# Kernel tuning notes

Hardware: AMD Instinct MI355X
Metric: run time of the kernel (lower is better)

The kernel has to match this reference:

```python
import math
import jax, jax.numpy as jnp
import numpy as np

B, T, D = 4, 2048, 1024
H = 16
HD = D // H  # 64

def setup_inputs() -> dict:
    key = jax.random.key(0)
    k1, k2, k3 = jax.random.split(key, 3)
    x = jax.random.normal(k1, (B, T, D), dtype=jnp.float32)
    # weights stored as [in, out]; equivalent to torch Linear weight [out,in] transposed
    w_qkv = jax.random.normal(k2, (D, 3 * D), dtype=jnp.float32) * (1.0 / math.sqrt(D))
    w_out = jax.random.normal(k3, (D, D), dtype=jnp.float32) * (1.0 / math.sqrt(D))
    return {"x": x, "w_qkv": w_qkv, "w_out": w_out}

def reference(x, w_qkv, w_out):
    b, t, c = x.shape
    hd = c // H
    qkv = x @ w_qkv                                   # [B,T,3C]
    q, k, v = jnp.split(qkv, 3, axis=-1)
    # [B,T,C] -> [B,H,T,hd]
    q = q.reshape(b, t, H, hd).transpose(0, 2, 1, 3)
    k = k.reshape(b, t, H, hd).transpose(0, 2, 1, 3)
    v = v.reshape(b, t, H, hd).transpose(0, 2, 1, 3)
    scale = 1.0 / math.sqrt(hd)
    scores = jnp.einsum('bhqd,bhkd->bhqk', q, k) * scale  # [B,H,T,T]
    causal = jnp.tril(jnp.ones((t, t), dtype=bool))
    scores = jnp.where(causal, scores, jnp.finfo(scores.dtype).min)
    attn = jax.nn.softmax(scores, axis=-1)
    out = jnp.einsum('bhqk,bhkd->bhqd', attn, v)       # [B,H,T,hd]
    out = out.transpose(0, 2, 1, 3).reshape(b, t, c)
    return out @ w_out
```

## Files before the change

### kernel.cpp

```cpp
#include <hip/hip_runtime.h>
#include <stdint.h>
#include <stddef.h>

#define BB 4
#define TT 2048
#define DD 1024
#define HH 16
#define HDIM 64
#define BT (BB*TT)
#define N1 (3*DD)

typedef __attribute__((ext_vector_type(8))) short short8;
typedef __attribute__((ext_vector_type(4))) float floatx4;
typedef __attribute__((ext_vector_type(4))) unsigned short ushortx4;

__device__ __forceinline__ unsigned short f2b(float f) {
    unsigned int u = __float_as_uint(f);
    u += 0x7fffu + ((u >> 16) & 1u);
    return (unsigned short)(u >> 16);
}

__device__ __forceinline__ void gld_lds16(const void* g, void* l) {
    __builtin_amdgcn_global_load_lds(
        (__attribute__((address_space(1))) void*)(g),
        (__attribute__((address_space(3))) void*)(l), 16, 0, 0);
}

__global__ void cvt_bf16(const float* __restrict__ src, unsigned short* __restrict__ dst, int n4) {
    int i = blockIdx.x * blockDim.x + threadIdx.x;
    if (i < n4) {
        floatx4 f = ((const floatx4*)src)[i];
        ushortx4 o;
        o.x = f2b(f.x); o.y = f2b(f.y); o.z = f2b(f.z); o.w = f2b(f.w);
        ((ushortx4*)dst)[i] = o;
    }
}

__global__ void transpose_cvt(const float* __restrict__ src, unsigned short* __restrict__ dst,
                              int R, int C) {
    __shared__ float tile[32][33];
    const int c0 = blockIdx.x * 32, r0 = blockIdx.y * 32;
    const int x = threadIdx.x, y = threadIdx.y;
    for (int yy = y; yy < 32; yy += 8)
        tile[yy][x] = src[(size_t)(r0 + yy) * C + c0 + x];
    __syncthreads();
    for (int yy = y; yy < 32; yy += 8)
        dst[(size_t)(c0 + yy) * R + r0 + x] = f2b(tile[x][yy]);
}

template<int MODE>
__global__ __launch_bounds__(256, 3)
void gemm_bt(const unsigned short* __restrict__ A,
             const unsigned short* __restrict__ Bt,
             void* __restrict__ Cout, int M, int N, int K,
             float qscale, unsigned short* __restrict__ vt_out) {
    __shared__ unsigned short a_tile[128 * 32];
    __shared__ unsigned short b_tile[128 * 32];
    const int tid  = threadIdx.x;
    const int wave = tid >> 6;
    const int lane = tid & 63;
    const int quad = lane >> 4;
    const int lc   = lane & 15;
    const int wm = wave >> 1, wn = wave & 1;
    const int row0 = blockIdx.y * 128;
    const int col0 = blockIdx.x * 128;

    const int c0 = wave, c1 = wave + 4;
    const int r_in = lane >> 2;
    const int kseg = (lane & 3) * 8;
    const unsigned short* gA0 = A  + (size_t)(row0 + c0 * 16 + r_in) * K + kseg;
    const unsigned short* gA1 = A  + (size_t)(row0 + c1 * 16 + r_in) * K + kseg;
    const unsigned short* gB0 = Bt + (size_t)(col0 + c0 * 16 + r_in) * K + kseg;
    const unsigned short* gB1 = Bt + (size_t)(col0 + c1 * 16 + r_in) * K + kseg;
    unsigned short* lA0 = &a_tile[c0 * 512];
    unsigned short* lA1 = &a_tile[c1 * 512];
    unsigned short* lB0 = &b_tile[c0 * 512];
    unsigned short* lB1 = &b_tile[c1 * 512];

    floatx4 acc[4][4];
    #pragma unroll
    for (int i = 0; i < 4; i++)
        #pragma unroll
        for (int j = 0; j < 4; j++)
            acc[i][j] = (floatx4){0.f, 0.f, 0.f, 0.f};

    const int nkt = K >> 5;
    for (int kt = 0; kt < nkt; ++kt) {
        __syncthreads();
        gld_lds16(gA0, lA0);
        gld_lds16(gA1, lA1);
        gld_lds16(gB0, lB0);
        gld_lds16(gB1, lB1);
        gA0 += 32; gA1 += 32; gB0 += 32; gB1 += 32;
        __syncthreads();

        short8 af[4], bf[4];
        #pragma unroll
        for (int mi = 0; mi < 4; ++mi)
            af[mi] = *(const short8*)&a_tile[(wm * 64 + mi * 16 + lc) * 32 + quad * 8];
        #pragma unroll
        for (int ni = 0; ni < 4; ++ni)
            bf[ni] = *(const short8*)&b_tile[(wn * 64 + ni * 16 + lc) * 32 + quad * 8];
        #pragma unroll
        for (int mi = 0; mi < 4; ++mi)
            #pragma unroll
            for (int ni = 0; ni < 4; ++ni)
                acc[mi][ni] = __builtin_amdgcn_mfma_f32_16x16x32_bf16(af[mi], bf[ni], acc[mi][ni], 0, 0, 0);
    }

    #pragma unroll
    for (int mi = 0; mi < 4; ++mi) {
        const int rbase = row0 + wm * 64 + mi * 16 + quad * 4;
        #pragma unroll
        for (int ni = 0; ni < 4; ++ni) {
            const int colbase = col0 + wn * 64 + ni * 16;
            const int col = colbase + lc;
            if (MODE == 0) {
                #pragma unroll
                for (int r = 0; r < 4; ++r)
                    ((float*)Cout)[(size_t)(rbase + r) * N + col] = acc[mi][ni][r];
            } else {
                if (colbase < 2 * DD) {
                    const float sc = (colbase < DD) ? qscale : 1.0f;
                    #pragma unroll
                    for (int r = 0; r < 4; ++r)
                        ((unsigned short*)Cout)[(size_t)(rbase + r) * N + col] = f2b(acc[mi][ni][r] * sc);
                } else {
                    const int vcol = col - 2 * DD;
                    const int hh = vcol >> 6, d = vcol & 63;
                    const int bq = rbase >> 11, t = rbase & 2047;
                    ushortx4 pk;
                    pk.x = f2b(acc[mi][ni][0]);
                    pk.y = f2b(acc[mi][ni][1]);
                    pk.z = f2b(acc[mi][ni][2]);
                    pk.w = f2b(acc[mi][ni][3]);
                    *(ushortx4*)&vt_out[(size_t)((bq * 16 + hh) * 64 + d) * TT + t] = pk;
                }
            }
        }
    }
}

__global__ __launch_bounds__(256, 2)
void attn_fwd(const unsigned short* __restrict__ qkv,
              const unsigned short* __restrict__ vt,
              unsigned short* __restrict__ out) {
    __shared__ unsigned short kbuf[2][64 * 64];
    __shared__ unsigned short vbuf[2][64 * 64];
    __shared__ unsigned short p_lds[4][32 * 72];
    const int bh = blockIdx.x;
    const int b = bh >> 4, h = bh & 15;
    const int pr = blockIdx.y;
    const int tid = threadIdx.x;
    const int wave = tid >> 6, lane = tid & 63;
    const int quad = lane >> 4, lc = lane & 15;
    unsigned short* pw = p_lds[wave];

    const int sr = wave * 8 + (lane >> 3);
    const int lg = (lane & 7) ^ (sr & 7);
    const unsigned short* ksrc0 = qkv + (size_t)(b * TT + sr) * N1 + DD + h * HDIM + lg * 8;
    const unsigned short* vsrc0 = vt + (size_t)(bh * HDIM + sr) * TT + lg * 8;
    const int stg = wave * 512;

    int fofs[4][2];
    #pragma unroll
    for (int mi = 0; mi < 4; ++mi)
        #pragma unroll
        for (int kk = 0; kk < 2; ++kk)
            fofs[mi][kk] = (mi * 16 + lc) * 64 + (((kk * 4 + quad) ^ (lc & 7)) * 8);

    gld_lds16(ksrc0, &kbuf[0][stg]);
    gld_lds16(ksrc0 + 32 * (size_t)N1, &kbuf[0][stg + 2048]);
    gld_lds16(vsrc0, &vbuf[0][stg]);
    gld_lds16(vsrc0 + 32 * (size_t)TT, &vbuf[0][stg + 2048]);
    int buf = 0;

    for (int pass = 0; pass < 2; ++pass) {
        const int j = pass ? (15 - pr) : pr;
        const int q0 = j * 128;
        const int r0 = q0 + wave * 32;
        const int tmax = 2 * j + 1;

        short8 qf[2][2];
        #pragma unroll
        for (int ni = 0; ni < 2; ++ni)
            #pragma unroll
            for (int kk = 0; kk < 2; ++kk)
                qf[ni][kk] = *(const short8*)(qkv + (size_t)(b * TT + r0 + ni * 16 + lc) * N1 + h * HDIM + kk * 32 + quad * 8);

        float lp[2] = {0.f, 0.f};
        floatx4 o_acc[4][2];
        #pragma unroll
        for (int mi = 0; mi < 4; ++mi)
            #pragma unroll
            for (int ni = 0; ni < 2; ++ni)
                o_acc[mi][ni] = (floatx4){0.f, 0.f, 0.f, 0.f};

        for (int t = 0; t <= tmax; ++t) {
            const int kv0 = t * 64;
            __syncthreads();

            const int nt = (t < tmax) ? (t + 1) : (pass == 0 ? 0 : -1);
            if (nt >= 0) {
                const unsigned short* ks = ksrc0 + (size_t)nt * 64 * N1;
                const unsigned short* vs = vsrc0 + nt * 64;
                gld_lds16(ks, &kbuf[buf ^ 1][stg]);
                gld_lds16(ks + 32 * (size_t)N1, &kbuf[buf ^ 1][stg + 2048]);
                gld_lds16(vs, &vbuf[buf ^ 1][stg]);
                gld_lds16(vs + 32 * (size_t)TT, &vbuf[buf ^ 1][stg + 2048]);
            }

            short8 kf[4][2];
            #pragma unroll
            for (int mi = 0; mi < 4; ++mi)
                #pragma unroll
                for (int kk = 0; kk < 2; ++kk)
                    kf[mi][kk] = *(const short8*)&kbuf[buf][fofs[mi][kk]];
            floatx4 sa[4][2];
            #pragma unroll
            for (int mi = 0; mi < 4; ++mi)
                #pragma unroll
                for (int ni = 0; ni < 2; ++ni) {
                    floatx4 z = (floatx4){0.f, 0.f, 0.f, 0.f};
                    z = __builtin_amdgcn_mfma_f32_16x16x32_bf16(kf[mi][0], qf[ni][0], z, 0, 0, 0);
                    z = __builtin_amdgcn_mfma_f32_16x16x32_bf16(kf[mi][1], qf[ni][1], z, 0, 0, 0);
                    sa[mi][ni] = z;
                }

            if (kv0 + 63 > r0) {
                #pragma unroll
                for (int ni = 0; ni < 2; ++ni) {
                    const int qg = r0 + ni * 16 + lc;
                    #pragma unroll
                    for (int mi = 0; mi < 4; ++mi) {
                        const int kvb = kv0 + mi * 16 + quad * 4;
                        #pragma unroll
                        for (int r = 0; r < 4; ++r)
                            sa[mi][ni][r] = (kvb + r <= qg) ? sa[mi][ni][r] : -1e30f;
                    }
                }
            }

            #pragma unroll
            for (int ni = 0; ni < 2; ++ni) {
                float rs = 0.f;
                #pragma unroll
                for (int mi = 0; mi < 4; ++mi) {
                    float p0 = __builtin_amdgcn_exp2f(sa[mi][ni][0]);
                    float p1 = __builtin_amdgcn_exp2f(sa[mi][ni][1]);
                    float p2 = __builtin_amdgcn_exp2f(sa[mi][ni][2]);
                    float p3 = __builtin_amdgcn_exp2f(sa[mi][ni][3]);
                    rs += (p0 + p1) + (p2 + p3);
                    ushortx4 pk;
                    pk.x = f2b(p0); pk.y = f2b(p1); pk.z = f2b(p2); pk.w = f2b(p3);
                    *(ushortx4*)&pw[(ni * 16 + lc) * 72 + mi * 16 + quad * 4] = pk;
                }
                lp[ni] += rs;
            }

            short8 pf[2][2];
            #pragma unroll
            for (int ni = 0; ni < 2; ++ni)
                #pragma unroll
                for (int kk = 0; kk < 2; ++kk)
                    pf[ni][kk] = *(const short8*)&pw[(ni * 16 + lc) * 72 + kk * 32 + quad * 8];
            short8 vf[4][2];
            #pragma unroll
            for (int mi = 0; mi < 4; ++mi)
                #pragma unroll
                for (int kk = 0; kk < 2; ++kk)
                    vf[mi][kk] = *(const short8*)&vbuf[buf][fofs[mi][kk]];
            #pragma unroll
            for (int mi = 0; mi < 4; ++mi)
                #pragma unroll
                for (int ni = 0; ni < 2; ++ni) {
                    o_acc[mi][ni] = __builtin_amdgcn_mfma_f32_16x16x32_bf16(vf[mi][0], pf[ni][0], o_acc[mi][ni], 0, 0, 0);
                    o_acc[mi][ni] = __builtin_amdgcn_mfma_f32_16x16x32_bf16(vf[mi][1], pf[ni][1], o_acc[mi][ni], 0, 0, 0);
                }

            buf ^= 1;
        }

        #pragma unroll
        for (int ni = 0; ni < 2; ++ni) {
            float lt = lp[ni];
            lt += __shfl_xor(lt, 16);
            lt += __shfl_xor(lt, 32);
            const float inv = 1.0f / lt;
            const size_t tok = (size_t)(b * TT + r0 + ni * 16 + lc);
            #pragma unroll
            for (int mi = 0; mi < 4; ++mi) {
                ushortx4 pk;
                pk.x = f2b(o_acc[mi][ni][0] * inv);
                pk.y = f2b(o_acc[mi][ni][1] * inv);
                pk.z = f2b(o_acc[mi][ni][2] * inv);
                pk.w = f2b(o_acc[mi][ni][3] * inv);
                *(ushortx4*)&out[tok * DD + h * HDIM + mi * 16 + quad * 4] = pk;
            }
        }
    }
}

extern "C" void kernel_launch(void* const* d_in, const int* in_sizes, int n_in,
                              void* d_out, int out_size, void* d_ws, size_t ws_size,
                              hipStream_t stream) {
    const float* x     = (const float*)d_in[0];
    const float* w_qkv = (const float*)d_in[1];
    const float* w_out = (const float*)d_in[2];
    float* out = (float*)d_out;

    unsigned short* ws  = (unsigned short*)d_ws;
    unsigned short* xb  = ws;
    unsigned short* qkv = xb  + (size_t)BT * DD;
    unsigned short* wqT = qkv + (size_t)BT * N1;
    unsigned short* woT = wqT + (size_t)N1 * DD;
    unsigned short* vtb = woT + (size_t)DD * DD;

    const float QSCALE = 0.18033688011112042f;

    cvt_bf16<<<(BT * DD / 4 + 255) / 256, 256, 0, stream>>>(x, xb, BT * DD / 4);
    transpose_cvt<<<dim3(N1 / 32, DD / 32), dim3(32, 8), 0, stream>>>(w_qkv, wqT, DD, N1);
    transpose_cvt<<<dim3(DD / 32, DD / 32), dim3(32, 8), 0, stream>>>(w_out, woT, DD, DD);
    gemm_bt<1><<<dim3(N1 / 128, BT / 128), 256, 0, stream>>>(xb, wqT, qkv, BT, N1, DD, QSCALE, vtb);
    attn_fwd<<<dim3(BB * HH, 8), 256, 0, stream>>>(qkv, vtb, xb);
    gemm_bt<0><<<dim3(DD / 128, BT / 128), 256, 0, stream>>>(xb, woT, out, BT, DD, DD, 1.0f, nullptr);
}
```

Before: 259.5 us.

## Double-buffer LDS tiles in bf16 GEMM to overlap global loads with MFMA

The GEMM's A and B shared-memory tiles become two-stage ping-pong buffers, and the first tile is prefetched before the K loop. Each iteration now issues the global-to-LDS loads for the next K slice into the other buffer, then runs MFMAs on the current one. This drops one barrier per iteration and aims to hide global load latency behind compute. In exchange, LDS use per block doubles, and the overlap can be lost if the compiler inserts a conservative vmcnt wait before the LDS reads.

```diff
diff --git a/kernel.cpp b/kernel.cpp
--- a/kernel.cpp
+++ b/kernel.cpp
@@ -54,8 +54,8 @@
              const unsigned short* __restrict__ Bt,
              void* __restrict__ Cout, int M, int N, int K,
              float qscale, unsigned short* __restrict__ vt_out) {
-    __shared__ unsigned short a_tile[128 * 32];
-    __shared__ unsigned short b_tile[128 * 32];
+    __shared__ unsigned short a_tile[2][128 * 32];
+    __shared__ unsigned short b_tile[2][128 * 32];
     const int tid  = threadIdx.x;
     const int wave = tid >> 6;
     const int lane = tid & 63;
@@ -72,10 +72,7 @@
     const unsigned short* gA1 = A  + (size_t)(row0 + c1 * 16 + r_in) * K + kseg;
     const unsigned short* gB0 = Bt + (size_t)(col0 + c0 * 16 + r_in) * K + kseg;
     const unsigned short* gB1 = Bt + (size_t)(col0 + c1 * 16 + r_in) * K + kseg;
-    unsigned short* lA0 = &a_tile[c0 * 512];
-    unsigned short* lA1 = &a_tile[c1 * 512];
-    unsigned short* lB0 = &b_tile[c0 * 512];
-    unsigned short* lB1 = &b_tile[c1 * 512];
+    const int sA0 = c0 * 512, sA1 = c1 * 512;
 
     floatx4 acc[4][4];
     #pragma unroll
@@ -84,28 +81,36 @@
         for (int j = 0; j < 4; j++)
             acc[i][j] = (floatx4){0.f, 0.f, 0.f, 0.f};
 
+    gld_lds16(gA0, &a_tile[0][sA0]);
+    gld_lds16(gA1, &a_tile[0][sA1]);
+    gld_lds16(gB0, &b_tile[0][sA0]);
+    gld_lds16(gB1, &b_tile[0][sA1]);
+    int buf = 0;
+
     const int nkt = K >> 5;
     for (int kt = 0; kt < nkt; ++kt) {
         __syncthreads();
-        gld_lds16(gA0, lA0);
-        gld_lds16(gA1, lA1);
-        gld_lds16(gB0, lB0);
-        gld_lds16(gB1, lB1);
-        gA0 += 32; gA1 += 32; gB0 += 32; gB1 += 32;
-        __syncthreads();
+        if (kt + 1 < nkt) {
+            gA0 += 32; gA1 += 32; gB0 += 32; gB1 += 32;
+            gld_lds16(gA0, &a_tile[buf ^ 1][sA0]);
+            gld_lds16(gA1, &a_tile[buf ^ 1][sA1]);
+            gld_lds16(gB0, &b_tile[buf ^ 1][sA0]);
+            gld_lds16(gB1, &b_tile[buf ^ 1][sA1]);
+        }
 
         short8 af[4], bf[4];
         #pragma unroll
         for (int mi = 0; mi < 4; ++mi)
-            af[mi] = *(const short8*)&a_tile[(wm * 64 + mi * 16 + lc) * 32 + quad * 8];
+            af[mi] = *(const short8*)&a_tile[buf][(wm * 64 + mi * 16 + lc) * 32 + quad * 8];
         #pragma unroll
         for (int ni = 0; ni < 4; ++ni)
-            bf[ni] = *(const short8*)&b_tile[(wn * 64 + ni * 16 + lc) * 32 + quad * 8];
+            bf[ni] = *(const short8*)&b_tile[buf][(wn * 64 + ni * 16 + lc) * 32 + quad * 8];
         #pragma unroll
         for (int mi = 0; mi < 4; ++mi)
             #pragma unroll
             for (int ni = 0; ni < 4; ++ni)
                 acc[mi][ni] = __builtin_amdgcn_mfma_f32_16x16x32_bf16(af[mi], bf[ni], acc[mi][ni], 0, 0, 0);
+        buf ^= 1;
     }
 
     #pragma unroll
```

After: 257.4 us. Within noise of the previous version (-0.8%).
